# Performance work log

Hardware: AMD Instinct MI355X
Metric: run time of the kernel (lower is better)

## Reference

```python
import jax, jax.numpy as jnp
import numpy as np

B, S, E, H = 8, 1024, 1024, 16
DK = E // H  # = n_wires = 64


def setup_inputs() -> dict:
    key = jax.random.key(0)
    k1, k2, k3 = jax.random.split(key, 3)
    x = jax.random.normal(k1, (B, S, E), dtype=jnp.float32)
    # trainable per-wire RX angles (shared across tokens and heads, as in QLayer)
    theta = jax.random.normal(k2, (DK,), dtype=jnp.float32)
    # combine_heads: nn.Linear(E, E, bias=False) -> weight [E, E], y = x @ W.T
    W_combine = (jax.random.normal(k3, (E, E), dtype=jnp.float32) / np.float32(np.sqrt(E)))
    return {"x": x, "theta": theta, "W_combine": W_combine}


def reference(x, theta, W_combine):
    # Quantum projection: per wire, RX(x_i) then RX(theta_i) on |0>, measure PauliZ.
    # RX(a)RX(b) = RX(a+b); <Z> of RX(a)|0> = cos(a)  =>  proj = cos(x + theta).
    b, s, e = x.shape
    xh = x.reshape(b, s, H, DK)            # [B, S, H, DK]
    proj = jnp.cos(xh + theta)             # product-state circuit, fully vectorized
    qkv = proj.transpose(0, 2, 1, 3)       # [B, H, S, DK]; q = k = v = proj

    scale = jnp.float32(1.0 / np.sqrt(DK))
    scores = jnp.einsum('bhqd,bhkd->bhqk', qkv, qkv) * scale  # [B, H, S, S]
    attn = jax.nn.softmax(scores, axis=-1)  # dropout disabled (eval / p=0)
    out = jnp.einsum('bhqk,bhkd->bhqd', attn, qkv)            # [B, H, S, DK]
    out = out.transpose(0, 2, 1, 3).reshape(b, s, e)          # [B, S, E]
    return out @ W_combine.T
```

## Files before the change

### kernel.cpp

```cpp
#include <hip/hip_runtime.h>
#include <hip/hip_bf16.h>
#include <stdint.h>

typedef float  f32x4   __attribute__((ext_vector_type(4)));
typedef float  f32x16  __attribute__((ext_vector_type(16)));
typedef __bf16 bf16x8  __attribute__((ext_vector_type(8)));
typedef __bf16 bf16x4  __attribute__((ext_vector_type(4)));

static constexpr int NB = 8, NS = 1024, NE = 1024, NH = 16;

#define MFMA16(a, b, c) __builtin_amdgcn_mfma_f32_16x16x32_bf16((a), (b), (c), 0, 0, 0)
#define MFMA32(a, b, c) __builtin_amdgcn_mfma_f32_32x32x16_bf16((a), (b), (c), 0, 0, 0)

__device__ __forceinline__ void gload_lds16(const void* g, void* l) {
    __builtin_amdgcn_global_load_lds(
        (const __attribute__((address_space(1))) void*)g,
        (__attribute__((address_space(3))) void*)l, 16, 0, 0);
}

__device__ __forceinline__ uint32_t cvt_pk_bf16(float lo, float hi) {
    uint32_t r;
    asm("v_cvt_pk_bf16_f32 %0, %1, %2" : "=v"(r) : "v"(lo), "v"(hi));
    return r;
}
__device__ __forceinline__ void pl32swap(uint32_t& a, uint32_t& b) {
    asm volatile("v_permlane32_swap_b32 %0, %1" : "+v"(a), "+v"(b));
}
__device__ __forceinline__ float exp2_raw(float x) {
    float r;
    asm("v_exp_f32 %0, %1" : "=v"(r) : "v"(x));
    return r;
}

__global__ __launch_bounds__(256) void k_proj(const float* __restrict__ x,
                                              const float* __restrict__ theta,
                                              __bf16* __restrict__ proj,
                                              __bf16* __restrict__ projT) {
    __shared__ float sm[64][65];
    const int bid  = blockIdx.x;
    const int bh   = bid >> 4;
    const int st0  = (bid & 15) << 6;
    const int b    = bh >> 4, h = bh & 15;
    const int t    = threadIdx.x;
    const int srow = t >> 2;
    const int j4   = t & 3;

    const float* xrow = x + ((size_t)(b * NS + st0 + srow)) * NE + h * 64;
    __bf16* prow = proj + ((size_t)bh * NS + st0 + srow) * 64;

#pragma unroll
    for (int k = 0; k < 4; ++k) {
        const int d = k * 16 + j4 * 4;
        float4 xv = *(const float4*)(xrow + d);
        float4 tv = *(const float4*)(theta + d);
        float c0 = __cosf(xv.x + tv.x);
        float c1 = __cosf(xv.y + tv.y);
        float c2 = __cosf(xv.z + tv.z);
        float c3 = __cosf(xv.w + tv.w);
        bf16x4 pv = {(__bf16)c0, (__bf16)c1, (__bf16)c2, (__bf16)c3};
        *(bf16x4*)(prow + d) = pv;
        sm[d + 0][srow] = c0;
        sm[d + 1][srow] = c1;
        sm[d + 2][srow] = c2;
        sm[d + 3][srow] = c3;
    }
    __syncthreads();

    const int drow = t >> 2;
    bf16x8 o0, o1;
#pragma unroll
    for (int i = 0; i < 8; ++i) {
        o0[i] = (__bf16)sm[drow][j4 * 16 + i];
        o1[i] = (__bf16)sm[drow][j4 * 16 + 8 + i];
    }
    __bf16* dst = projT + ((size_t)bh * 64 + drow) * NS + st0 + j4 * 16;
    *(bf16x8*)dst = o0;
    *(bf16x8*)(dst + 8) = o1;
}

__global__ __launch_bounds__(256) void k_cvtW(const float* __restrict__ W,
                                              __bf16* __restrict__ Wb) {
    const int i = (blockIdx.x * 256 + threadIdx.x) * 4;
    float4 v = *(const float4*)(W + i);
    bf16x4 o = {(__bf16)v.x, (__bf16)v.y, (__bf16)v.z, (__bf16)v.w};
    *(bf16x4*)(Wb + i) = o;
}

__global__ __launch_bounds__(256, 2) void k_attn(const __bf16* __restrict__ proj,
                                                 const __bf16* __restrict__ projT,
                                                 __bf16* __restrict__ attn_out) {
    __shared__ __align__(16) char smem[32768];
    __bf16* const smK0 = (__bf16*)(smem);
    __bf16* const smV0 = (__bf16*)(smem + 8192);
    __bf16* const smK1 = (__bf16*)(smem + 16384);
    __bf16* const smV1 = (__bf16*)(smem + 24576);

    const int bid  = blockIdx.x;
    const int bh   = (bid & 7) + 8 * ((bid >> 3) & 15);
    const int qblk = bid >> 7;
    const int t    = threadIdx.x;
    const int w    = t >> 6;
    const int lane = t & 63;
    const int hi   = lane >> 5;
    const int l5   = lane & 31;
    const int l7   = l5 & 7;
    const int qw   = qblk * 256 + w * 64;
    const int b    = bh >> 4, h = bh & 15;

    const __bf16* P  = proj  + (size_t)bh * NS * 64;
    const __bf16* PT = projT + (size_t)bh * 64 * NS;

    const float csc = 0.18033688f;

    bf16x8 bq[2][4];
#pragma unroll
    for (int q01 = 0; q01 < 2; ++q01)
#pragma unroll
        for (int d = 0; d < 4; ++d)
            bq[q01][d] = *(const bf16x8*)(P + (size_t)(qw + q01 * 32 + l5) * 64 + d * 16 + hi * 8);

    int roff[4];
#pragma unroll
    for (int d = 0; d < 4; ++d) roff[d] = l5 * 64 + ((d * 2 + hi) ^ l7) * 8;

    const int srow  = t >> 3;
    const int sjsrc = (t & 7) ^ (srow & 7);
    char* const dK0 = (char*)smK0 + t * 16;
    char* const dV0 = (char*)smV0 + t * 16;
    char* const dK1 = (char*)smK1 + t * 16;
    char* const dV1 = (char*)smV1 + t * 16;

#define STAGE(kvoff, dk, dv)                                                           \
    do {                                                                               \
        gload_lds16(P  + (size_t)((kvoff) + srow)      * 64 + sjsrc * 8, (dk));        \
        gload_lds16(P  + (size_t)((kvoff) + 32 + srow) * 64 + sjsrc * 8, (dk) + 4096); \
        gload_lds16(PT + (size_t)srow        * NS + (kvoff) + sjsrc * 8, (dv));        \
        gload_lds16(PT + (size_t)(32 + srow) * NS + (kvoff) + sjsrc * 8, (dv) + 4096); \
    } while (0)

    f32x16 acc0[2], acc1[2];
#pragma unroll
    for (int dt = 0; dt < 2; ++dt) {
        acc0[dt] = (f32x16){0.f,0.f,0.f,0.f,0.f,0.f,0.f,0.f,0.f,0.f,0.f,0.f,0.f,0.f,0.f,0.f};
        acc1[dt] = (f32x16){0.f,0.f,0.f,0.f,0.f,0.f,0.f,0.f,0.f,0.f,0.f,0.f,0.f,0.f,0.f,0.f};
    }
    float rs0 = 0.f, rs1 = 0.f;

    auto computeTile = [&](const __bf16* kB, const __bf16* vB) {
#pragma unroll
        for (int kt = 0; kt < 2; ++kt) {
            bf16x8 ak[4];
#pragma unroll
            for (int d = 0; d < 4; ++d)
                ak[d] = *(const bf16x8*)(kB + roff[d] + kt * 2048);

            f32x16 st0 = (f32x16){0.f,0.f,0.f,0.f,0.f,0.f,0.f,0.f,0.f,0.f,0.f,0.f,0.f,0.f,0.f,0.f};
            f32x16 st1 = (f32x16){0.f,0.f,0.f,0.f,0.f,0.f,0.f,0.f,0.f,0.f,0.f,0.f,0.f,0.f,0.f,0.f};
            __builtin_amdgcn_s_setprio(1);
#pragma unroll
            for (int d = 0; d < 4; ++d) {
                st0 = MFMA32(ak[d], bq[0][d], st0);
                st1 = MFMA32(ak[d], bq[1][d], st1);
            }
            __builtin_amdgcn_s_setprio(0);

            uint32_t c0[8], c1[8];
            {
                float p[16];
#pragma unroll
                for (int r = 0; r < 16; ++r) p[r] = exp2_raw(st0[r] * csc);
                rs0 += (((p[0] + p[1]) + (p[2] + p[3])) + ((p[4] + p[5]) + (p[6] + p[7]))) +
                       (((p[8] + p[9]) + (p[10] + p[11])) + ((p[12] + p[13]) + (p[14] + p[15])));
#pragma unroll
                for (int j = 0; j < 8; ++j) c0[j] = cvt_pk_bf16(p[2 * j], p[2 * j + 1]);
            }
            {
                float p[16];
#pragma unroll
                for (int r = 0; r < 16; ++r) p[r] = exp2_raw(st1[r] * csc);
                rs1 += (((p[0] + p[1]) + (p[2] + p[3])) + ((p[4] + p[5]) + (p[6] + p[7]))) +
                       (((p[8] + p[9]) + (p[10] + p[11])) + ((p[12] + p[13]) + (p[14] + p[15])));
#pragma unroll
                for (int j = 0; j < 8; ++j) c1[j] = cvt_pk_bf16(p[2 * j], p[2 * j + 1]);
            }
            pl32swap(c0[0], c0[2]); pl32swap(c0[1], c0[3]);
            pl32swap(c0[4], c0[6]); pl32swap(c0[5], c0[7]);
            pl32swap(c1[0], c1[2]); pl32swap(c1[1], c1[3]);
            pl32swap(c1[4], c1[6]); pl32swap(c1[5], c1[7]);

#pragma unroll
            for (int half = 0; half < 2; ++half) {
                const int ks = kt * 2 + half;
                union U4 { uint32_t u[4]; bf16x8 v; };
                U4 f0, f1;
#pragma unroll
                for (int j = 0; j < 4; ++j) {
                    f0.u[j] = c0[half * 4 + j];
                    f1.u[j] = c1[half * 4 + j];
                }
                __builtin_amdgcn_s_setprio(1);
#pragma unroll
                for (int dt = 0; dt < 2; ++dt) {
                    bf16x8 av = *(const bf16x8*)(vB + roff[ks] + dt * 2048);
                    acc0[dt] = MFMA32(av, f0.v, acc0[dt]);
                    acc1[dt] = MFMA32(av, f1.v, acc1[dt]);
                }
                __builtin_amdgcn_s_setprio(0);
            }
        }
    };

    STAGE(0, dK0, dV0);
    __syncthreads();

#pragma unroll 1
    for (int it2 = 0; it2 < 8; ++it2) {
        STAGE((2 * it2 + 1) * 64, dK1, dV1);
        computeTile(smK0, smV0);
        __syncthreads();
        if (it2 < 7) STAGE((2 * it2 + 2) * 64, dK0, dV0);
        computeTile(smK1, smV1);
        __syncthreads();
    }
#undef STAGE

    float* const epw = (float*)smem + w * (32 * 33);
    const int orow = lane >> 1;
    const int ohalf = lane & 1;

#pragma unroll
    for (int q01 = 0; q01 < 2; ++q01) {
        float rs = (q01 == 0) ? rs0 : rs1;
        rs += __shfl_xor(rs, 32);
        const float inv = 1.0f / rs;
#pragma unroll
        for (int dt = 0; dt < 2; ++dt) {
            const f32x16 a = (q01 == 0) ? acc0[dt] : acc1[dt];
#pragma unroll
            for (int r = 0; r < 16; ++r)
                epw[l5 * 33 + (r & 3) + 8 * (r >> 2) + 4 * hi] = a[r] * inv;
            bf16x8 o0, o1;
#pragma unroll
            for (int i = 0; i < 8; ++i) {
                o0[i] = (__bf16)(epw[orow * 33 + ohalf * 16 + i]);
                o1[i] = (__bf16)(epw[orow * 33 + ohalf * 16 + 8 + i]);
            }
            __bf16* dst = attn_out +
                ((size_t)b * NS + qblk * 256 + w * 64 + q01 * 32 + orow) * NE +
                h * 64 + dt * 32 + ohalf * 16;
            *(bf16x8*)dst = o0;
            *(bf16x8*)(dst + 8) = o1;
        }
    }
}

__global__ __launch_bounds__(256, 2) void k_gemm(const __bf16* __restrict__ A,
                                                 const __bf16* __restrict__ Bw,
                                                 float* __restrict__ C) {
    constexpr int K = 1024, N = 1024;
    __shared__ __align__(16) __bf16 As[2][128 * 64];
    __shared__ __align__(16) __bf16 Bs[2][128 * 64];

    const int t = threadIdx.x;
    const int lane = t & 63, w = t >> 6;
    const int g = lane >> 4, c = lane & 15;
    const int wr = w >> 1, wc = w & 1;
    const size_t row0 = (size_t)blockIdx.x * 128;
    const size_t col0 = (size_t)blockIdx.y * 128;

    const __bf16* Ag = A  + row0 * K;
    const __bf16* Bg = Bw + col0 * K;

    const int srow = t >> 3;
    const int sj   = (t & 7) ^ (srow & 7);

#define GSTAGE(kb, buf)                                                           \
    do {                                                                          \
        _Pragma("unroll")                                                         \
        for (int p = 0; p < 4; ++p) {                                             \
            gload_lds16(Ag + (size_t)(p * 32 + srow) * K + (kb) + sj * 8,         \
                        (char*)&As[buf][0] + p * 4096 + t * 16);                  \
            gload_lds16(Bg + (size_t)(p * 32 + srow) * K + (kb) + sj * 8,         \
                        (char*)&Bs[buf][0] + p * 4096 + t * 16);                  \
        }                                                                         \
    } while (0)

    f32x4 acc[4][4];
#pragma unroll
    for (int m = 0; m < 4; ++m)
#pragma unroll
        for (int n = 0; n < 4; ++n) acc[m][n] = (f32x4){0.f, 0.f, 0.f, 0.f};

    const int c7 = c & 7;

    auto computeBuf = [&](int buf) {
#pragma unroll
        for (int ks = 0; ks < 2; ++ks) {
            bf16x8 a[4], bfr[4];
#pragma unroll
            for (int m = 0; m < 4; ++m)
                a[m] = *(const bf16x8*)(&As[buf][(wr * 64 + m * 16 + c) * 64 +
                                                 ((ks * 4 + g) ^ c7) * 8]);
#pragma unroll
            for (int n = 0; n < 4; ++n)
                bfr[n] = *(const bf16x8*)(&Bs[buf][(wc * 64 + n * 16 + c) * 64 +
                                                   ((ks * 4 + g) ^ c7) * 8]);
#pragma unroll
            for (int m = 0; m < 4; ++m)
#pragma unroll
                for (int n = 0; n < 4; ++n) acc[m][n] = MFMA16(a[m], bfr[n], acc[m][n]);
        }
    };

    GSTAGE(0, 0);
    __syncthreads();

#pragma unroll 1
    for (int kt = 0; kt < 8; ++kt) {
        GSTAGE(kt * 128 + 64, 1);
        computeBuf(0);
        __syncthreads();
        if (kt < 7) GSTAGE(kt * 128 + 128, 0);
        computeBuf(1);
        __syncthreads();
    }
#undef GSTAGE

#pragma unroll
    for (int m = 0; m < 4; ++m)
#pragma unroll
        for (int n = 0; n < 4; ++n)
#pragma unroll
            for (int r = 0; r < 4; ++r)
                C[(row0 + wr * 64 + m * 16 + 4 * g + r) * N + col0 + wc * 64 + n * 16 + c] =
                    acc[m][n][r];
}

extern "C" void kernel_launch(void* const* d_in, const int* in_sizes, int n_in,
                              void* d_out, int out_size, void* d_ws, size_t ws_size,
                              hipStream_t stream) {
    const float* x     = (const float*)d_in[0];
    const float* theta = (const float*)d_in[1];
    const float* W     = (const float*)d_in[2];
    float* out = (float*)d_out;

    char* ws = (char*)d_ws;
    __bf16* proj  = (__bf16*)(ws);
    __bf16* projT = (__bf16*)(ws + 16777216);
    __bf16* Wb    = (__bf16*)(ws + 33554432);
    __bf16* ao    = (__bf16*)(ws + 35651584);

    k_cvtW<<<(NE * NE / 4) / 256, 256, 0, stream>>>(W, Wb);
    k_proj<<<NB * NH * (NS / 64), 256, 0, stream>>>(x, theta, proj, projT);
    k_attn<<<NB * NH * 4, 256, 0, stream>>>(proj, projT, ao);
    dim3 gg(NB * NS / 128, NE / 128);
    k_gemm<<<gg, 256, 0, stream>>>(ao, Wb, out);
}
```

Baseline: 84.47 us.

## Split attention KV sequence across two wave groups with LDS reduction

Doubles the attention block to 512 threads: two groups of four waves each process half of the key/value sequence for the same query tiles, with separate double-buffered LDS sets. At the end, the second group dumps its partial accumulators and row sums into LDS, and the first group adds them and writes the normalized output. This halves the serial KV loop per wave to add latency hiding, at the cost of double the LDS footprint, an extra reduction pass with two barriers, and possibly fewer resident blocks per CU.

```diff
diff --git a/kernel.cpp b/kernel.cpp
--- a/kernel.cpp
+++ b/kernel.cpp
@@ -86,26 +86,24 @@
     *(bf16x4*)(Wb + i) = o;
 }
 
-__global__ __launch_bounds__(256, 2) void k_attn(const __bf16* __restrict__ proj,
+__global__ __launch_bounds__(512, 4) void k_attn(const __bf16* __restrict__ proj,
                                                  const __bf16* __restrict__ projT,
                                                  __bf16* __restrict__ attn_out) {
-    __shared__ __align__(16) char smem[32768];
-    __bf16* const smK0 = (__bf16*)(smem);
-    __bf16* const smV0 = (__bf16*)(smem + 8192);
-    __bf16* const smK1 = (__bf16*)(smem + 16384);
-    __bf16* const smV1 = (__bf16*)(smem + 24576);
+    __shared__ __align__(16) char smem[65536 + 2048];
 
     const int bid  = blockIdx.x;
     const int bh   = (bid & 7) + 8 * ((bid >> 3) & 15);
     const int qblk = bid >> 7;
     const int t    = threadIdx.x;
-    const int w    = t >> 6;
+    const int wv   = t >> 6;
     const int lane = t & 63;
     const int hi   = lane >> 5;
     const int l5   = lane & 31;
     const int l7   = l5 & 7;
-    const int qw   = qblk * 256 + w * 64;
-    const int b    = bh >> 4, h = bh & 15;
+    const int qtile = wv & 3;
+    const int kvh   = wv >> 2;
+    const int qw    = qblk * 256 + qtile * 64;
+    const int b     = bh >> 4, h = bh & 15;
 
     const __bf16* P  = proj  + (size_t)bh * NS * 64;
     const __bf16* PT = projT + (size_t)bh * 64 * NS;
@@ -119,23 +117,30 @@
         for (int d = 0; d < 4; ++d)
             bq[q01][d] = *(const bf16x8*)(P + (size_t)(qw + q01 * 32 + l5) * 64 + d * 16 + hi * 8);
 
+    char* const setb = smem + kvh * 32768;
+    const __bf16* const smK[2] = {(const __bf16*)(setb), (const __bf16*)(setb + 16384)};
+    const __bf16* const smV[2] = {(const __bf16*)(setb + 8192), (const __bf16*)(setb + 24576)};
+
     int roff[4];
 #pragma unroll
     for (int d = 0; d < 4; ++d) roff[d] = l5 * 64 + ((d * 2 + hi) ^ l7) * 8;
 
-    const int srow  = t >> 3;
-    const int sjsrc = (t & 7) ^ (srow & 7);
-    char* const dK0 = (char*)smK0 + t * 16;
-    char* const dV0 = (char*)smV0 + t * 16;
-    char* const dK1 = (char*)smK1 + t * 16;
-    char* const dV1 = (char*)smV1 + t * 16;
-
-#define STAGE(kvoff, dk, dv)                                                           \
-    do {                                                                               \
-        gload_lds16(P  + (size_t)((kvoff) + srow)      * 64 + sjsrc * 8, (dk));        \
-        gload_lds16(P  + (size_t)((kvoff) + 32 + srow) * 64 + sjsrc * 8, (dk) + 4096); \
-        gload_lds16(PT + (size_t)srow        * NS + (kvoff) + sjsrc * 8, (dv));        \
-        gload_lds16(PT + (size_t)(32 + srow) * NS + (kvoff) + sjsrc * 8, (dv) + 4096); \
+    const int ts    = t & 255;
+    const int kvadd = (t >> 8) * 512;
+    const int srow  = ts >> 3;
+    const int sjsrc = (ts & 7) ^ (srow & 7);
+    char* const dK0 = setb + ts * 16;
+    char* const dV0 = setb + 8192 + ts * 16;
+    char* const dK1 = setb + 16384 + ts * 16;
+    char* const dV1 = setb + 24576 + ts * 16;
+
+#define STAGE(tile, dk, dv)                                                                  \
+    do {                                                                                     \
+        const int kvo = kvadd + (tile) * 64;                                                 \
+        gload_lds16(P  + (size_t)(kvo + srow)      * 64 + sjsrc * 8, (dk));                  \
+        gload_lds16(P  + (size_t)(kvo + 32 + srow) * 64 + sjsrc * 8, (dk) + 4096);           \
+        gload_lds16(PT + (size_t)srow        * NS + kvo + sjsrc * 8, (dv));                  \
+        gload_lds16(PT + (size_t)(32 + srow) * NS + kvo + sjsrc * 8, (dv) + 4096);           \
     } while (0)
 
     f32x16 acc0[2], acc1[2];
@@ -214,42 +219,81 @@
     __syncthreads();
 
 #pragma unroll 1
-    for (int it2 = 0; it2 < 8; ++it2) {
-        STAGE((2 * it2 + 1) * 64, dK1, dV1);
-        computeTile(smK0, smV0);
+    for (int it2 = 0; it2 < 4; ++it2) {
+        STAGE(2 * it2 + 1, dK1, dV1);
+        computeTile(smK[0], smV[0]);
         __syncthreads();
-        if (it2 < 7) STAGE((2 * it2 + 2) * 64, dK0, dV0);
-        computeTile(smK1, smV1);
+        if (it2 < 3) STAGE(2 * it2 + 2, dK0, dV0);
+        computeTile(smK[1], smV[1]);
         __syncthreads();
     }
 #undef STAGE
 
-    float* const epw = (float*)smem + w * (32 * 33);
-    const int orow = lane >> 1;
-    const int ohalf = lane & 1;
-
-#pragma unroll
-    for (int q01 = 0; q01 < 2; ++q01) {
-        float rs = (q01 == 0) ? rs0 : rs1;
-        rs += __shfl_xor(rs, 32);
-        const float inv = 1.0f / rs;
-#pragma unroll
-        for (int dt = 0; dt < 2; ++dt) {
-            const f32x16 a = (q01 == 0) ? acc0[dt] : acc1[dt];
-#pragma unroll
-            for (int r = 0; r < 16; ++r)
-                epw[l5 * 33 + (r & 3) + 8 * (r >> 2) + 4 * hi] = a[r] * inv;
-            bf16x8 o0, o1;
-#pragma unroll
-            for (int i = 0; i < 8; ++i) {
-                o0[i] = (__bf16)(epw[orow * 33 + ohalf * 16 + i]);
-                o1[i] = (__bf16)(epw[orow * 33 + ohalf * 16 + 8 + i]);
-            }
-            __bf16* dst = attn_out +
-                ((size_t)b * NS + qblk * 256 + w * 64 + q01 * 32 + orow) * NE +
-                h * 64 + dt * 32 + ohalf * 16;
-            *(bf16x8*)dst = o0;
-            *(bf16x8*)(dst + 8) = o1;
+    float* const dmp = (float*)smem;
+    float* const rsd = (float*)(smem + 65536);
+    if (kvh == 1) {
+#pragma unroll
+        for (int q01 = 0; q01 < 2; ++q01)
+#pragma unroll
+            for (int dt = 0; dt < 2; ++dt) {
+                const f32x16 a = (q01 == 0) ? acc0[dt] : acc1[dt];
+#pragma unroll
+                for (int r4 = 0; r4 < 4; ++r4) {
+                    f32x4 qd = {a[r4 * 4 + 0], a[r4 * 4 + 1], a[r4 * 4 + 2], a[r4 * 4 + 3]};
+                    *(f32x4*)(dmp + qtile * 4096 + ((q01 * 2 + dt) * 4 + r4) * 256 + lane * 4) = qd;
+                }
+            }
+        rsd[qtile * 128 + lane * 2]     = rs0;
+        rsd[qtile * 128 + lane * 2 + 1] = rs1;
+    }
+    __syncthreads();
+    if (kvh == 0) {
+#pragma unroll
+        for (int q01 = 0; q01 < 2; ++q01)
+#pragma unroll
+            for (int dt = 0; dt < 2; ++dt) {
+                f32x16& a = (q01 == 0) ? acc0[dt] : acc1[dt];
+#pragma unroll
+                for (int r4 = 0; r4 < 4; ++r4) {
+                    f32x4 qd = *(const f32x4*)(dmp + qtile * 4096 +
+                                               ((q01 * 2 + dt) * 4 + r4) * 256 + lane * 4);
+                    a[r4 * 4 + 0] += qd[0]; a[r4 * 4 + 1] += qd[1];
+                    a[r4 * 4 + 2] += qd[2]; a[r4 * 4 + 3] += qd[3];
+                }
+            }
+        rs0 += rsd[qtile * 128 + lane * 2];
+        rs1 += rsd[qtile * 128 + lane * 2 + 1];
+    }
+    __syncthreads();
+
+    if (kvh == 0) {
+        float* const epw = (float*)smem + qtile * (32 * 33);
+        const int orow = lane >> 1;
+        const int ohalf = lane & 1;
+
+#pragma unroll
+        for (int q01 = 0; q01 < 2; ++q01) {
+            float rs = (q01 == 0) ? rs0 : rs1;
+            rs += __shfl_xor(rs, 32);
+            const float inv = 1.0f / rs;
+#pragma unroll
+            for (int dt = 0; dt < 2; ++dt) {
+                const f32x16 a = (q01 == 0) ? acc0[dt] : acc1[dt];
+#pragma unroll
+                for (int r = 0; r < 16; ++r)
+                    epw[l5 * 33 + (r & 3) + 8 * (r >> 2) + 4 * hi] = a[r] * inv;
+                bf16x8 o0, o1;
+#pragma unroll
+                for (int i = 0; i < 8; ++i) {
+                    o0[i] = (__bf16)(epw[orow * 33 + ohalf * 16 + i]);
+                    o1[i] = (__bf16)(epw[orow * 33 + ohalf * 16 + 8 + i]);
+                }
+                __bf16* dst = attn_out +
+                    ((size_t)b * NS + qblk * 256 + qtile * 64 + q01 * 32 + orow) * NE +
+                    h * 64 + dt * 32 + ohalf * 16;
+                *(bf16x8*)dst = o0;
+                *(bf16x8*)(dst + 8) = o1;
+            }
         }
     }
 }
@@ -352,7 +396,7 @@
 
     k_cvtW<<<(NE * NE / 4) / 256, 256, 0, stream>>>(W, Wb);
     k_proj<<<NB * NH * (NS / 64), 256, 0, stream>>>(x, theta, proj, projT);
-    k_attn<<<NB * NH * 4, 256, 0, stream>>>(proj, projT, ao);
+    k_attn<<<NB * NH * 4, 512, 0, stream>>>(proj, projT, ao);
     dim3 gg(NB * NS / 128, NE / 128);
     k_gemm<<<gg, 256, 0, stream>>>(ao, Wb, out);
 }
```

New measurement: 300.2 us. 255% more time.

## Merge W conversion into projection kernel and retile output GEMM to 64x128

Applied to the files above, without the earlier changes.

The separate weight-conversion kernel is folded into the projection kernel as extra trailing blocks, which removes one launch. The output GEMM is retiled from 128x128 tiles with K-step 64 to 64x128 tiles with K-step 32, with a new XOR swizzle and launch bounds raised to 4 blocks per SM. The grid is reordered so blocks that share a row tile sit next to each other, and MFMA sections run at raised wave priority. Smaller tiles give more blocks and higher occupancy for the 1024-block grid, but each block reuses less data and the K loop has twice as many barriers.

```diff
diff --git a/kernel.cpp b/kernel.cpp
--- a/kernel.cpp
+++ b/kernel.cpp
@@ -35,13 +35,24 @@
 __global__ __launch_bounds__(256) void k_proj(const float* __restrict__ x,
                                               const float* __restrict__ theta,
                                               __bf16* __restrict__ proj,
-                                              __bf16* __restrict__ projT) {
+                                              __bf16* __restrict__ projT,
+                                              const float* __restrict__ W,
+                                              __bf16* __restrict__ Wb) {
     __shared__ float sm[64][65];
-    const int bid  = blockIdx.x;
+    const int bid = blockIdx.x;
+    const int t   = threadIdx.x;
+
+    if (bid >= 2048) {
+        const int i = ((bid - 2048) * 256 + t) * 4;
+        float4 v = *(const float4*)(W + i);
+        bf16x4 o = {(__bf16)v.x, (__bf16)v.y, (__bf16)v.z, (__bf16)v.w};
+        *(bf16x4*)(Wb + i) = o;
+        return;
+    }
+
     const int bh   = bid >> 4;
     const int st0  = (bid & 15) << 6;
     const int b    = bh >> 4, h = bh & 15;
-    const int t    = threadIdx.x;
     const int srow = t >> 2;
     const int j4   = t & 3;
 
@@ -78,14 +89,6 @@
     *(bf16x8*)(dst + 8) = o1;
 }
 
-__global__ __launch_bounds__(256) void k_cvtW(const float* __restrict__ W,
-                                              __bf16* __restrict__ Wb) {
-    const int i = (blockIdx.x * 256 + threadIdx.x) * 4;
-    float4 v = *(const float4*)(W + i);
-    bf16x4 o = {(__bf16)v.x, (__bf16)v.y, (__bf16)v.z, (__bf16)v.w};
-    *(bf16x4*)(Wb + i) = o;
-}
-
 __global__ __launch_bounds__(256, 2) void k_attn(const __bf16* __restrict__ proj,
                                                  const __bf16* __restrict__ projT,
                                                  __bf16* __restrict__ attn_out) {
@@ -254,85 +257,83 @@
     }
 }
 
-__global__ __launch_bounds__(256, 2) void k_gemm(const __bf16* __restrict__ A,
+__global__ __launch_bounds__(256, 4) void k_gemm(const __bf16* __restrict__ A,
                                                  const __bf16* __restrict__ Bw,
                                                  float* __restrict__ C) {
     constexpr int K = 1024, N = 1024;
-    __shared__ __align__(16) __bf16 As[2][128 * 64];
-    __shared__ __align__(16) __bf16 Bs[2][128 * 64];
+    __shared__ __align__(16) __bf16 As[2][64 * 32];
+    __shared__ __align__(16) __bf16 Bs[2][128 * 32];
 
     const int t = threadIdx.x;
     const int lane = t & 63, w = t >> 6;
     const int g = lane >> 4, c = lane & 15;
     const int wr = w >> 1, wc = w & 1;
-    const size_t row0 = (size_t)blockIdx.x * 128;
-    const size_t col0 = (size_t)blockIdx.y * 128;
+    const size_t row0 = (size_t)blockIdx.y * 64;
+    const size_t col0 = (size_t)blockIdx.x * 128;
 
     const __bf16* Ag = A  + row0 * K;
     const __bf16* Bg = Bw + col0 * K;
 
-    const int srow = t >> 3;
-    const int sj   = (t & 7) ^ (srow & 7);
-
-#define GSTAGE(kb, buf)                                                           \
-    do {                                                                          \
-        _Pragma("unroll")                                                         \
-        for (int p = 0; p < 4; ++p) {                                             \
-            gload_lds16(Ag + (size_t)(p * 32 + srow) * K + (kb) + sj * 8,         \
-                        (char*)&As[buf][0] + p * 4096 + t * 16);                  \
-            gload_lds16(Bg + (size_t)(p * 32 + srow) * K + (kb) + sj * 8,         \
-                        (char*)&Bs[buf][0] + p * 4096 + t * 16);                  \
-        }                                                                         \
+    const int srow = t >> 2;
+    const int sj   = (t & 3) ^ ((srow >> 1) & 3);
+
+#define GSTAGE(kb, buf)                                                          \
+    do {                                                                         \
+        gload_lds16(Ag + (size_t)srow * K + (kb) + sj * 8,                       \
+                    (char*)&As[buf][0] + t * 16);                                \
+        gload_lds16(Bg + (size_t)srow * K + (kb) + sj * 8,                       \
+                    (char*)&Bs[buf][0] + t * 16);                                \
+        gload_lds16(Bg + (size_t)(64 + srow) * K + (kb) + sj * 8,                \
+                    (char*)&Bs[buf][0] + 4096 + t * 16);                         \
     } while (0)
 
-    f32x4 acc[4][4];
-#pragma unroll
-    for (int m = 0; m < 4; ++m)
+    f32x4 acc[2][4];
+#pragma unroll
+    for (int m = 0; m < 2; ++m)
 #pragma unroll
         for (int n = 0; n < 4; ++n) acc[m][n] = (f32x4){0.f, 0.f, 0.f, 0.f};
 
-    const int c7 = c & 7;
-
     auto computeBuf = [&](int buf) {
-#pragma unroll
-        for (int ks = 0; ks < 2; ++ks) {
-            bf16x8 a[4], bfr[4];
-#pragma unroll
-            for (int m = 0; m < 4; ++m)
-                a[m] = *(const bf16x8*)(&As[buf][(wr * 64 + m * 16 + c) * 64 +
-                                                 ((ks * 4 + g) ^ c7) * 8]);
-#pragma unroll
-            for (int n = 0; n < 4; ++n)
-                bfr[n] = *(const bf16x8*)(&Bs[buf][(wc * 64 + n * 16 + c) * 64 +
-                                                   ((ks * 4 + g) ^ c7) * 8]);
-#pragma unroll
-            for (int m = 0; m < 4; ++m)
-#pragma unroll
-                for (int n = 0; n < 4; ++n) acc[m][n] = MFMA16(a[m], bfr[n], acc[m][n]);
+        bf16x8 a[2], bfr[4];
+#pragma unroll
+        for (int m = 0; m < 2; ++m) {
+            const int row = wr * 32 + m * 16 + c;
+            a[m] = *(const bf16x8*)(&As[buf][row * 32 + (g ^ ((row >> 1) & 3)) * 8]);
         }
+#pragma unroll
+        for (int n = 0; n < 4; ++n) {
+            const int row = wc * 64 + n * 16 + c;
+            bfr[n] = *(const bf16x8*)(&Bs[buf][row * 32 + (g ^ ((row >> 1) & 3)) * 8]);
+        }
+        __builtin_amdgcn_s_setprio(1);
+#pragma unroll
+        for (int m = 0; m < 2; ++m)
+#pragma unroll
+            for (int n = 0; n < 4; ++n) acc[m][n] = MFMA16(a[m], bfr[n], acc[m][n]);
+        __builtin_amdgcn_s_setprio(0);
     };
 
     GSTAGE(0, 0);
     __syncthreads();
 
 #pragma unroll 1
-    for (int kt = 0; kt < 8; ++kt) {
-        GSTAGE(kt * 128 + 64, 1);
+    for (int kt = 0; kt < 16; ++kt) {
+        GSTAGE(kt * 64 + 32, 1);
         computeBuf(0);
         __syncthreads();
-        if (kt < 7) GSTAGE(kt * 128 + 128, 0);
+        if (kt < 15) GSTAGE(kt * 64 + 64, 0);
         computeBuf(1);
         __syncthreads();
     }
 #undef GSTAGE
 
 #pragma unroll
-    for (int m = 0; m < 4; ++m)
+    for (int m = 0; m < 2; ++m)
 #pragma unroll
         for (int n = 0; n < 4; ++n)
 #pragma unroll
             for (int r = 0; r < 4; ++r)
-                C[(row0 + wr * 64 + m * 16 + 4 * g + r) * N + col0 + wc * 64 + n * 16 + c] =
+                C[(row0 + wr * 32 + m * 16 + 4 * g + r) * N + col0 + wc * 64 + n * 16 + c] =
                     acc[m][n][r];
 }
 
@@ -350,9 +351,9 @@
     __bf16* Wb    = (__bf16*)(ws + 33554432);
     __bf16* ao    = (__bf16*)(ws + 35651584);
 
-    k_cvtW<<<(NE * NE / 4) / 256, 256, 0, stream>>>(W, Wb);
-    k_proj<<<NB * NH * (NS / 64), 256, 0, stream>>>(x, theta, proj, projT);
+    k_proj<<<NB * NH * (NS / 64) + (NE * NE / 4) / 256, 256, 0, stream>>>(
+        x, theta, proj, projT, W, Wb);
     k_attn<<<NB * NH * 4, 256, 0, stream>>>(proj, projT, ao);
-    dim3 gg(NB * NS / 128, NE / 128);
+    dim3 gg(NE / 128, NB * NS / 64);
     k_gemm<<<gg, 256, 0, stream>>>(ao, Wb, out);
 }
```

New measurement: 86.80 us. 1.03x slower.
